# Optimization experiments

Measured on AMD Instinct MI355X. Metric: run time of the kernel, lower is better.

The kernel has to match this reference:

```python
import jax, jax.numpy as jnp
import numpy as np

B, T, H, S, K, V = 64, 2048, 512, 512, 128, 128
EPS = 1e-12  # F.normalize default eps


def setup_inputs() -> dict:
    key = jax.random.key(0)
    ks = jax.random.split(key, 9)
    scale_s = 1.0 / np.sqrt(S)
    scale_h = 1.0 / np.sqrt(H)
    return {
        "decoder_state": jax.random.normal(ks[0], (B, S), jnp.float32),
        "listener_output": jax.random.normal(ks[1], (B, T, H), jnp.float32),
        "outputs_length": jax.random.randint(ks[2], (B,), 1, T + 1, jnp.int32),
        "Ws": jax.random.uniform(ks[3], (K, S), jnp.float32, -scale_s, scale_s),
        "bs": jax.random.uniform(ks[4], (K,), jnp.float32, -scale_s, scale_s),
        "Wh": jax.random.uniform(ks[5], (K, H), jnp.float32, -scale_h, scale_h),
        "bh": jax.random.uniform(ks[6], (K,), jnp.float32, -scale_h, scale_h),
        "Wv": jax.random.uniform(ks[7], (V, H), jnp.float32, -scale_h, scale_h),
        "bv": jax.random.uniform(ks[8], (V,), jnp.float32, -scale_h, scale_h),
    }


def reference(decoder_state, listener_output, outputs_length, Ws, bs, Wh, bh, Wv, bv):
    # query: (B, K); key: (B, T, K)
    query = decoder_state @ Ws.T + bs
    keys = jnp.einsum('bth,kh->btk', listener_output, Wh) + bh
    energy = jnp.einsum('bk,btk->bt', query, keys)          # (B, T)
    attention = jax.nn.softmax(energy, axis=-1)
    # mask: positions >= outputs_length[i] zeroed, EXCEPT sample i == 0 (original loop skips i==0)
    t_idx = jnp.arange(T)
    valid = t_idx[None, :] < outputs_length[:, None]        # (B, T)
    valid = valid.at[0].set(True)
    mask = valid.astype(attention.dtype)
    attention = attention * mask
    # L1 normalize over time (F.normalize p=1, dim=2)
    denom = jnp.maximum(jnp.sum(jnp.abs(attention), axis=-1, keepdims=True), EPS)
    attention = attention / denom
    value = jnp.einsum('bth,vh->btv', listener_output, Wv) + bv  # (B, T, V)
    value = value * mask[:, :, None]
    context = jnp.einsum('bt,btv->bv', attention, value)     # (B, V)
    return context, attention[:, None, :]
```

## Files before the change

kernel.cpp:

```cpp
#include <hip/hip_runtime.h>
#include <hip/hip_bf16.h>

#define B 64
#define T 2048
#define H 512
#define S 512
#define K 128
#define V 128
#define SPLITS 16
#define TPS (T / SPLITS)

__global__ __launch_bounds__(256) void prep_kernel(
    const float* __restrict__ dec, const float* __restrict__ Ws,
    const float* __restrict__ bs, const float* __restrict__ Wh,
    const float* __restrict__ bh, float* __restrict__ wq,
    float* __restrict__ cb) {
  const int b = blockIdx.x;
  const int tid = threadIdx.x;
  __shared__ float s_dec[S];
  __shared__ float s_q[K];

  for (int i = tid; i < S; i += 256) s_dec[i] = dec[b * S + i];
  __syncthreads();

  if (tid < K) {
    const float* w = Ws + (size_t)tid * S;
    float acc = bs[tid];
    #pragma unroll 4
    for (int s = 0; s < S; s++) acc += w[s] * s_dec[s];
    s_q[tid] = acc;
  }
  __syncthreads();

  if (tid == 0) {
    float c = 0.f;
    for (int k = 0; k < K; k++) c += s_q[k] * bh[k];
    cb[b] = c;
  }
  for (int h = tid; h < H; h += 256) {
    float acc = 0.f;
    #pragma unroll 4
    for (int k = 0; k < K; k++) acc += s_q[k] * Wh[(size_t)k * H + h];
    wq[b * H + h] = acc;
  }
}

__global__ __launch_bounds__(256) void energy_kernel(
    const float* __restrict__ L, const float* __restrict__ wq,
    const float* __restrict__ cb, float* __restrict__ energy) {
  const int b = blockIdx.x >> 6;
  const int tc = blockIdx.x & 63;
  const int lane = threadIdx.x & 63;
  const int wave = threadIdx.x >> 6;

  const float4 q0 = *(const float4*)(wq + b * H + lane * 8);
  const float4 q1 = *(const float4*)(wq + b * H + lane * 8 + 4);
  const float c = cb[b];
  const float* Lb = L + (size_t)b * T * H;

  #pragma unroll
  for (int i = 0; i < 8; i++) {
    const int t = tc * 32 + wave * 8 + i;
    const float* row = Lb + (size_t)t * H + lane * 8;
    const float4 a0 = *(const float4*)(row);
    const float4 a1 = *(const float4*)(row + 4);
    float d = a0.x * q0.x + a0.y * q0.y + a0.z * q0.z + a0.w * q0.w +
              a1.x * q1.x + a1.y * q1.y + a1.z * q1.z + a1.w * q1.w;
    #pragma unroll
    for (int off = 32; off > 0; off >>= 1) d += __shfl_xor(d, off);
    if (lane == 0) energy[b * T + t] = d + c;
  }
}

__global__ __launch_bounds__(256) void softmax_kernel(
    const float* __restrict__ energy, const int* __restrict__ len,
    float* __restrict__ att) {
  const int b = blockIdx.x;
  const int tid = threadIdx.x;
  const int lane = tid & 63;
  const int wave = tid >> 6;
  const int lb = (b == 0) ? T : len[b];

  float e[8];
  bool v[8];
  float m = -1e30f;
  #pragma unroll
  for (int i = 0; i < 8; i++) {
    const int t = tid + 256 * i;
    e[i] = energy[b * T + t];
    v[i] = (t < lb);
    if (v[i]) m = fmaxf(m, e[i]);
  }
  #pragma unroll
  for (int off = 32; off > 0; off >>= 1) m = fmaxf(m, __shfl_xor(m, off));
  __shared__ float sm[4];
  __shared__ float sl[4];
  if (lane == 0) sm[wave] = m;
  __syncthreads();
  m = fmaxf(fmaxf(sm[0], sm[1]), fmaxf(sm[2], sm[3]));

  float w[8];
  float l = 0.f;
  #pragma unroll
  for (int i = 0; i < 8; i++) {
    w[i] = v[i] ? __expf(e[i] - m) : 0.f;
    l += w[i];
  }
  #pragma unroll
  for (int off = 32; off > 0; off >>= 1) l += __shfl_xor(l, off);
  if (lane == 0) sl[wave] = l;
  __syncthreads();
  l = sl[0] + sl[1] + sl[2] + sl[3];
  const float inv = 1.0f / fmaxf(l, 1e-12f);
  #pragma unroll
  for (int i = 0; i < 8; i++) att[b * T + tid + 256 * i] = w[i] * inv;
}

__global__ __launch_bounds__(256) void ctx_partial_kernel(
    const float* __restrict__ L, const float* __restrict__ att,
    float* __restrict__ partials) {
  const int b = blockIdx.x >> 4;
  const int sp = blockIdx.x & (SPLITS - 1);
  const int tid = threadIdx.x;
  const int t0 = sp * TPS;

  __shared__ float s_w[TPS];
  for (int i = tid; i < TPS; i += 256) s_w[i] = att[b * T + t0 + i];
  __syncthreads();

  const float* Lp = L + (size_t)b * T * H + (size_t)t0 * H + tid * 2;
  float2 acc = {0.f, 0.f};
  #pragma unroll 4
  for (int t = 0; t < TPS; t++) {
    const float wv = s_w[t];
    const float2 x = *(const float2*)(Lp + (size_t)t * H);
    acc.x += wv * x.x;
    acc.y += wv * x.y;
  }
  *(float2*)(partials + ((size_t)(b * SPLITS + sp)) * H + tid * 2) = acc;
}

__global__ __launch_bounds__(256) void finalize_kernel(
    const float* __restrict__ partials, const float* __restrict__ Wv,
    const float* __restrict__ bv, float* __restrict__ ctx_out) {
  const int b = blockIdx.x;
  const int tid = threadIdx.x;
  __shared__ float s_ctx[H];

  float2 acc = {0.f, 0.f};
  #pragma unroll
  for (int sp = 0; sp < SPLITS; sp++) {
    const float2 p =
        *(const float2*)(partials + ((size_t)(b * SPLITS + sp)) * H + tid * 2);
    acc.x += p.x;
    acc.y += p.y;
  }
  s_ctx[tid * 2] = acc.x;
  s_ctx[tid * 2 + 1] = acc.y;
  __syncthreads();

  if (tid < V) {
    const float* w = Wv + (size_t)tid * H;
    float a = bv[tid];
    #pragma unroll 4
    for (int h = 0; h < H; h += 4) {
      a += w[h] * s_ctx[h] + w[h + 1] * s_ctx[h + 1] + w[h + 2] * s_ctx[h + 2] +
           w[h + 3] * s_ctx[h + 3];
    }
    ctx_out[b * V + tid] = a;
  }
}

extern "C" void kernel_launch(void* const* d_in, const int* in_sizes, int n_in,
                              void* d_out, int out_size, void* d_ws,
                              size_t ws_size, hipStream_t stream) {
  const float* dec = (const float*)d_in[0];
  const float* L   = (const float*)d_in[1];
  const int*   len = (const int*)d_in[2];
  const float* Ws  = (const float*)d_in[3];
  const float* bs  = (const float*)d_in[4];
  const float* Wh  = (const float*)d_in[5];
  const float* bh  = (const float*)d_in[6];
  const float* Wv  = (const float*)d_in[7];
  const float* bv  = (const float*)d_in[8];

  float* ctx_out = (float*)d_out;
  float* att_out = (float*)d_out + B * V;

  float* ws = (float*)d_ws;
  float* wq = ws;
  float* cb = wq + B * H;
  float* energy = cb + B;
  float* partials = energy + B * T;

  prep_kernel<<<B, 256, 0, stream>>>(dec, Ws, bs, Wh, bh, wq, cb);
  energy_kernel<<<B * (T / 32), 256, 0, stream>>>(L, wq, cb, energy);
  softmax_kernel<<<B, 256, 0, stream>>>(energy, len, att_out);
  ctx_partial_kernel<<<B * SPLITS, 256, 0, stream>>>(L, att_out, partials);
  finalize_kernel<<<B, 256, 0, stream>>>(partials, Wv, bv, ctx_out);
}
```

Baseline: 481.3 us.

## Fuse energy, online softmax and context accumulation into one pass over listener output

Replaces the separate energy, softmax and context-partial kernels with a single split-T kernel. It computes each energy dot product and keeps a flash-style online softmax with running max, sum and weighted context accumulators, so the listener output is read once instead of twice. It also skips rows at or beyond each sample's valid length, avoiding reads of masked timesteps. A combine kernel merges the per-split max, sum and context, and a separate kernel rewrites normalized attention from the stored energies. In exchange, each wave runs a serial per-row loop with a shuffle reduction and rescaling.

```diff
diff --git a/kernel.cpp b/kernel.cpp
--- a/kernel.cpp
+++ b/kernel.cpp
@@ -7,8 +7,10 @@
 #define S 512
 #define K 128
 #define V 128
-#define SPLITS 16
-#define TPS (T / SPLITS)
+#define SPL 16
+#define RPB (T / SPL)
+#define RPW (RPB / 4)
+#define PSTRIDE 516
 
 __global__ __launch_bounds__(256) void prep_kernel(
     const float* __restrict__ dec, const float* __restrict__ Ws,
@@ -45,118 +47,120 @@
   }
 }
 
-__global__ __launch_bounds__(256) void energy_kernel(
+__global__ __launch_bounds__(256) void fused_kernel(
     const float* __restrict__ L, const float* __restrict__ wq,
-    const float* __restrict__ cb, float* __restrict__ energy) {
-  const int b = blockIdx.x >> 6;
-  const int tc = blockIdx.x & 63;
+    const float* __restrict__ cb, const int* __restrict__ len,
+    float* __restrict__ energy, float* __restrict__ partials) {
+  const int b = blockIdx.x >> 4;
+  const int sp = blockIdx.x & (SPL - 1);
   const int lane = threadIdx.x & 63;
   const int wave = threadIdx.x >> 6;
-
-  const float4 q0 = *(const float4*)(wq + b * H + lane * 8);
-  const float4 q1 = *(const float4*)(wq + b * H + lane * 8 + 4);
-  const float c = cb[b];
-  const float* Lb = L + (size_t)b * T * H;
-
-  #pragma unroll
-  for (int i = 0; i < 8; i++) {
-    const int t = tc * 32 + wave * 8 + i;
-    const float* row = Lb + (size_t)t * H + lane * 8;
-    const float4 a0 = *(const float4*)(row);
-    const float4 a1 = *(const float4*)(row + 4);
-    float d = a0.x * q0.x + a0.y * q0.y + a0.z * q0.z + a0.w * q0.w +
-              a1.x * q1.x + a1.y * q1.y + a1.z * q1.z + a1.w * q1.w;
-    #pragma unroll
-    for (int off = 32; off > 0; off >>= 1) d += __shfl_xor(d, off);
-    if (lane == 0) energy[b * T + t] = d + c;
-  }
-}
-
-__global__ __launch_bounds__(256) void softmax_kernel(
-    const float* __restrict__ energy, const int* __restrict__ len,
-    float* __restrict__ att) {
+  const int tid = threadIdx.x;
+  const int lb = (b == 0) ? T : len[b];
+
+  __shared__ float s_ctx[4][H];
+  __shared__ float s_ml[4][2];
+
+  const int h0 = lane * 4;
+  float m = -__builtin_huge_valf();
+  float lsum = 0.f;
+  float4 acc0 = {0.f, 0.f, 0.f, 0.f};
+  float4 acc1 = {0.f, 0.f, 0.f, 0.f};
+
+  const int start = sp * RPB + wave * RPW;
+  const int end = min(start + RPW, lb);
+
+  if (start < end) {
+    const float4 q0 = *(const float4*)(wq + b * H + h0);
+    const float4 q1 = *(const float4*)(wq + b * H + 256 + h0);
+    const float c = cb[b];
+    const float* Lr = L + ((size_t)b * T + start) * H;
+    for (int r = start; r < end; r++, Lr += H) {
+      const float4 a0 = *(const float4*)(Lr + h0);
+      const float4 a1 = *(const float4*)(Lr + 256 + h0);
+      float d = a0.x * q0.x + a0.y * q0.y + a0.z * q0.z + a0.w * q0.w +
+                a1.x * q1.x + a1.y * q1.y + a1.z * q1.z + a1.w * q1.w;
+      #pragma unroll
+      for (int off = 32; off > 0; off >>= 1) d += __shfl_xor(d, off);
+      const float e = d + c;
+      if (lane == 0) energy[b * T + r] = e;
+      if (e > m) {
+        const float s = __expf(m - e);
+        lsum *= s;
+        acc0.x *= s; acc0.y *= s; acc0.z *= s; acc0.w *= s;
+        acc1.x *= s; acc1.y *= s; acc1.z *= s; acc1.w *= s;
+        m = e;
+      }
+      const float w = __expf(e - m);
+      lsum += w;
+      acc0.x += w * a0.x; acc0.y += w * a0.y;
+      acc0.z += w * a0.z; acc0.w += w * a0.w;
+      acc1.x += w * a1.x; acc1.y += w * a1.y;
+      acc1.z += w * a1.z; acc1.w += w * a1.w;
+    }
+  }
+
+  if (lane == 0) { s_ml[wave][0] = m; s_ml[wave][1] = lsum; }
+  *(float4*)&s_ctx[wave][h0] = acc0;
+  *(float4*)&s_ctx[wave][256 + h0] = acc1;
+  __syncthreads();
+
+  const float M = fmaxf(fmaxf(s_ml[0][0], s_ml[1][0]),
+                        fmaxf(s_ml[2][0], s_ml[3][0]));
+  float sc[4], ltot = 0.f;
+  #pragma unroll
+  for (int w = 0; w < 4; w++) {
+    sc[w] = (s_ml[w][0] > -1e38f) ? __expf(s_ml[w][0] - M) : 0.f;
+    ltot += s_ml[w][1] * sc[w];
+  }
+  float v0 = 0.f, v1 = 0.f;
+  #pragma unroll
+  for (int w = 0; w < 4; w++) {
+    v0 += s_ctx[w][tid * 2] * sc[w];
+    v1 += s_ctx[w][tid * 2 + 1] * sc[w];
+  }
+  float* part = partials + (size_t)blockIdx.x * PSTRIDE;
+  *(float2*)(part + tid * 2) = make_float2(v0, v1);
+  if (tid == 0) { part[512] = M; part[513] = ltot; }
+}
+
+__global__ __launch_bounds__(256) void combine_kernel(
+    const float* __restrict__ partials, const float* __restrict__ Wv,
+    const float* __restrict__ bv, float* __restrict__ ctx_out,
+    float* __restrict__ Mv, float* __restrict__ Iv) {
   const int b = blockIdx.x;
   const int tid = threadIdx.x;
-  const int lane = tid & 63;
-  const int wave = tid >> 6;
-  const int lb = (b == 0) ? T : len[b];
-
-  float e[8];
-  bool v[8];
-  float m = -1e30f;
-  #pragma unroll
-  for (int i = 0; i < 8; i++) {
-    const int t = tid + 256 * i;
-    e[i] = energy[b * T + t];
-    v[i] = (t < lb);
-    if (v[i]) m = fmaxf(m, e[i]);
-  }
-  #pragma unroll
-  for (int off = 32; off > 0; off >>= 1) m = fmaxf(m, __shfl_xor(m, off));
-  __shared__ float sm[4];
-  __shared__ float sl[4];
-  if (lane == 0) sm[wave] = m;
-  __syncthreads();
-  m = fmaxf(fmaxf(sm[0], sm[1]), fmaxf(sm[2], sm[3]));
-
-  float w[8];
-  float l = 0.f;
-  #pragma unroll
-  for (int i = 0; i < 8; i++) {
-    w[i] = v[i] ? __expf(e[i] - m) : 0.f;
-    l += w[i];
-  }
-  #pragma unroll
-  for (int off = 32; off > 0; off >>= 1) l += __shfl_xor(l, off);
-  if (lane == 0) sl[wave] = l;
-  __syncthreads();
-  l = sl[0] + sl[1] + sl[2] + sl[3];
-  const float inv = 1.0f / fmaxf(l, 1e-12f);
-  #pragma unroll
-  for (int i = 0; i < 8; i++) att[b * T + tid + 256 * i] = w[i] * inv;
-}
-
-__global__ __launch_bounds__(256) void ctx_partial_kernel(
-    const float* __restrict__ L, const float* __restrict__ att,
-    float* __restrict__ partials) {
-  const int b = blockIdx.x >> 4;
-  const int sp = blockIdx.x & (SPLITS - 1);
-  const int tid = threadIdx.x;
-  const int t0 = sp * TPS;
-
-  __shared__ float s_w[TPS];
-  for (int i = tid; i < TPS; i += 256) s_w[i] = att[b * T + t0 + i];
-  __syncthreads();
-
-  const float* Lp = L + (size_t)b * T * H + (size_t)t0 * H + tid * 2;
-  float2 acc = {0.f, 0.f};
+  __shared__ float s_ml[SPL][2];
+  __shared__ float s_ctx[H];
+
+  if (tid < SPL) {
+    const float* p = partials + (size_t)(b * SPL + tid) * PSTRIDE;
+    s_ml[tid][0] = p[512];
+    s_ml[tid][1] = p[513];
+  }
+  __syncthreads();
+
+  float M = -__builtin_huge_valf();
+  #pragma unroll
+  for (int sp = 0; sp < SPL; sp++) M = fmaxf(M, s_ml[sp][0]);
+  float sc[SPL], ltot = 0.f;
+  #pragma unroll
+  for (int sp = 0; sp < SPL; sp++) {
+    sc[sp] = (s_ml[sp][0] > -1e38f) ? __expf(s_ml[sp][0] - M) : 0.f;
+    ltot += s_ml[sp][1] * sc[sp];
+  }
+  const float inv = 1.0f / fmaxf(ltot, 1e-12f);
+
+  float v0 = 0.f, v1 = 0.f;
   #pragma unroll 4
-  for (int t = 0; t < TPS; t++) {
-    const float wv = s_w[t];
-    const float2 x = *(const float2*)(Lp + (size_t)t * H);
-    acc.x += wv * x.x;
-    acc.y += wv * x.y;
-  }
-  *(float2*)(partials + ((size_t)(b * SPLITS + sp)) * H + tid * 2) = acc;
-}
-
-__global__ __launch_bounds__(256) void finalize_kernel(
-    const float* __restrict__ partials, const float* __restrict__ Wv,
-    const float* __restrict__ bv, float* __restrict__ ctx_out) {
-  const int b = blockIdx.x;
-  const int tid = threadIdx.x;
-  __shared__ float s_ctx[H];
-
-  float2 acc = {0.f, 0.f};
-  #pragma unroll
-  for (int sp = 0; sp < SPLITS; sp++) {
-    const float2 p =
-        *(const float2*)(partials + ((size_t)(b * SPLITS + sp)) * H + tid * 2);
-    acc.x += p.x;
-    acc.y += p.y;
-  }
-  s_ctx[tid * 2] = acc.x;
-  s_ctx[tid * 2 + 1] = acc.y;
+  for (int sp = 0; sp < SPL; sp++) {
+    const float* p = partials + (size_t)(b * SPL + sp) * PSTRIDE;
+    v0 += p[tid * 2] * sc[sp];
+    v1 += p[tid * 2 + 1] * sc[sp];
+  }
+  s_ctx[tid * 2] = v0 * inv;
+  s_ctx[tid * 2 + 1] = v1 * inv;
+  if (tid == 0) { Mv[b] = M; Iv[b] = inv; }
   __syncthreads();
 
   if (tid < V) {
@@ -164,10 +168,27 @@
     float a = bv[tid];
     #pragma unroll 4
     for (int h = 0; h < H; h += 4) {
-      a += w[h] * s_ctx[h] + w[h + 1] * s_ctx[h + 1] + w[h + 2] * s_ctx[h + 2] +
-           w[h + 3] * s_ctx[h + 3];
+      a += w[h] * s_ctx[h] + w[h + 1] * s_ctx[h + 1] +
+           w[h + 2] * s_ctx[h + 2] + w[h + 3] * s_ctx[h + 3];
     }
     ctx_out[b * V + tid] = a;
+  }
+}
+
+__global__ __launch_bounds__(256) void attwrite_kernel(
+    const float* __restrict__ energy, const int* __restrict__ len,
+    const float* __restrict__ Mv, const float* __restrict__ Iv,
+    float* __restrict__ att) {
+  const int b = blockIdx.x;
+  const int tid = threadIdx.x;
+  const int lb = (b == 0) ? T : len[b];
+  const float M = Mv[b];
+  const float inv = Iv[b];
+  #pragma unroll
+  for (int i = 0; i < 8; i++) {
+    const int t = tid + 256 * i;
+    const float e = (t < lb) ? energy[b * T + t] : M;
+    att[b * T + t] = (t < lb) ? __expf(e - M) * inv : 0.f;
   }
 }
 
@@ -192,10 +213,11 @@
   float* cb = wq + B * H;
   float* energy = cb + B;
   float* partials = energy + B * T;
+  float* Mv = partials + B * SPL * PSTRIDE;
+  float* Iv = Mv + B;
 
   prep_kernel<<<B, 256, 0, stream>>>(dec, Ws, bs, Wh, bh, wq, cb);
-  energy_kernel<<<B * (T / 32), 256, 0, stream>>>(L, wq, cb, energy);
-  softmax_kernel<<<B, 256, 0, stream>>>(energy, len, att_out);
-  ctx_partial_kernel<<<B * SPLITS, 256, 0, stream>>>(L, att_out, partials);
-  finalize_kernel<<<B, 256, 0, stream>>>(partials, Wv, bv, ctx_out);
-}
+  fused_kernel<<<B * SPL, 256, 0, stream>>>(L, wq, cb, len, energy, partials);
+  combine_kernel<<<B, 256, 0, stream>>>(partials, Wv, bv, ctx_out, Mv, Iv);
+  attwrite_kernel<<<B, 256, 0, stream>>>(energy, len, Mv, Iv, att_out);
+}
```

Result: faster. 421.7 us (-12.4%).
